# Kernel optimization log

Measured on AMD Instinct MI355X. Metric: run time of the kernel, lower is better.

The kernel has to match this reference:

```python
import jax, jax.numpy as jnp
import numpy as np

N_GENE = 4762
N_CELL = 847


def _graph_conv(x_src, src, dst, n_src, n_dst, W, b):
    """DGL GraphConv with norm='both': D_src^{-1/2} A D_dst^{-1/2} X W + b."""
    ones_e = jnp.ones(src.shape, jnp.float32)
    deg_out = jax.ops.segment_sum(ones_e, src, num_segments=n_src)
    norm_src = jnp.clip(deg_out, 1.0, None) ** -0.5
    feat = x_src * norm_src[:, None]            # [n_src, d]
    msg = feat[src]                              # gather  [E, d]
    agg = jax.ops.segment_sum(msg, dst, num_segments=n_dst)  # scatter-add [n_dst, d]
    deg_in = jax.ops.segment_sum(ones_e, dst, num_segments=n_dst)
    norm_dst = jnp.clip(deg_in, 1.0, None) ** -0.5
    return (agg * norm_dst[:, None]) @ W + b


def setup_inputs() -> dict:
    key = jax.random.key(0)
    ks = jax.random.split(key, 12)
    E = 200000
    d = 256
    inp = {
        "gene_emb": jax.random.normal(ks[0], (N_GENE, d), jnp.float32),
        "cell_emb": jax.random.normal(ks[1], (N_CELL, d), jnp.float32),
        "W_g2c": jax.random.normal(ks[2], (d, d), jnp.float32) * (1.0 / np.sqrt(d)),
        "b_g2c": jnp.zeros((d,), jnp.float32),
        "W_c2g": jax.random.normal(ks[3], (d, d), jnp.float32) * (1.0 / np.sqrt(d)),
        "b_c2g": jnp.zeros((d,), jnp.float32),
        "Wp": jax.random.normal(ks[4], (2 * d, 1), jnp.float32) * (1.0 / np.sqrt(2 * d)),
        "bp": jnp.zeros((1,), jnp.float32),
        "g2c_src": jax.random.randint(ks[5], (E,), 0, N_GENE, jnp.int32),
        "g2c_dst": jax.random.randint(ks[6], (E,), 0, N_CELL, jnp.int32),
        "c2g_src": jax.random.randint(ks[7], (E,), 0, N_CELL, jnp.int32),
        "c2g_dst": jax.random.randint(ks[8], (E,), 0, N_GENE, jnp.int32),
        "dec_src": jax.random.randint(ks[9], (E,), 0, N_GENE, jnp.int32),
        "dec_dst": jax.random.randint(ks[10], (E,), 0, N_CELL, jnp.int32),
    }
    return inp


def reference(gene_emb, cell_emb, W_g2c, b_g2c, W_c2g, b_c2g, Wp, bp,
              g2c_src, g2c_dst, c2g_src, c2g_dst, dec_src, dec_dst):
    # HeteroGraphConv (aggregate='sum'): each dst type receives from one relation here.
    h_cell = _graph_conv(gene_emb, g2c_src, g2c_dst, N_GENE, N_CELL, W_g2c, b_g2c)
    h_gene = _graph_conv(cell_emb, c2g_src, c2g_dst, N_CELL, N_GENE, W_c2g, b_c2g)
    h_gene = jax.nn.relu(h_gene)
    h_cell = jax.nn.relu(h_cell)
    # HeteroMLPPredictor: concat(src_h, dst_h) @ Wp + bp on dec_graph edges.
    x = jnp.concatenate([h_gene[dec_src], h_cell[dec_dst]], axis=1)  # [E_dec, 512]
    score = x @ Wp + bp                                               # [E_dec, 1]
    return (score, h_gene, h_cell)
```

## Files before the change

kernel.cpp:

```cpp
#include <hip/hip_runtime.h>

#define N_GENE 4762
#define N_CELL 847
#define NEDGE  200000
#define D      256
#define NPART  64

typedef __attribute__((ext_vector_type(8))) short short8;
typedef __attribute__((ext_vector_type(8))) unsigned short ushort8v;
typedef __attribute__((ext_vector_type(4))) float f32x4;

#define S_G_OUT 0
#define S_C_IN  (S_G_OUT + N_GENE)
#define S_C_OUT (S_C_IN + N_CELL)
#define S_G_IN  (S_C_OUT + N_CELL)
#define NBINS   (S_G_IN + N_GENE)

#define ALIGN8(x) (((x) + 7) & ~7)

#define A_DEG      0
#define A_NRM      (A_DEG + NBINS)
#define A_OFFS_C   (A_NRM + NBINS)
#define A_OFFS_G   (A_OFFS_C + N_CELL + 1)
#define A_SORT_C   ALIGN8(A_OFFS_G + N_GENE + 1)
#define A_SORT_G   (A_SORT_C + 2 * NEDGE)
#define A_PART     (A_SORT_G + 2 * NEDGE)
#define A_SG       (A_PART + NPART * NBINS)
#define A_SC       (A_SG + N_GENE)
#define A_GENE_BF  ALIGN8(A_SC + N_CELL)
#define A_CELL_BF  ALIGN8(A_GENE_BF + N_GENE * D / 2)
#define A_WT1_BF   ALIGN8(A_CELL_BF + N_CELL * D / 2)
#define A_WT2_BF   ALIGN8(A_WT1_BF + D * D / 2)
#define A_AGGC_BF  ALIGN8(A_WT2_BF + D * D / 2)
#define A_AGGG_BF  ALIGN8(A_AGGC_BF + N_CELL * D / 2)

__device__ __forceinline__ unsigned short f2bf(float f) {
    unsigned u = __float_as_uint(f);
    u = (u + 0x7FFFu + ((u >> 16) & 1u)) >> 16;
    return (unsigned short)u;
}
__device__ __forceinline__ float bf2f(unsigned short b) {
    return __uint_as_float(((unsigned)b) << 16);
}

__global__ __launch_bounds__(1024) void k_pre(
        const int* __restrict__ g2c_src, const int* __restrict__ g2c_dst,
        const int* __restrict__ c2g_src, const int* __restrict__ c2g_dst,
        const float* __restrict__ gene_emb, const float* __restrict__ cell_emb,
        const float* __restrict__ W_g2c, const float* __restrict__ W_c2g,
        int* __restrict__ partial,
        unsigned short* __restrict__ gene_bf, unsigned short* __restrict__ cell_bf,
        unsigned short* __restrict__ wt1, unsigned short* __restrict__ wt2,
        float* __restrict__ sg, float* __restrict__ sc) {
    __shared__ int sh[N_GENE];
    int B = blockIdx.x, T = threadIdx.x;
    if (B < 4 * NPART) {
        int grp = B >> 6, blk = B & (NPART - 1);
        const int* idx;
        int segbase, segn;
        if      (grp == 0) { idx = g2c_src; segbase = S_G_OUT; segn = N_GENE; }
        else if (grp == 1) { idx = g2c_dst; segbase = S_C_IN;  segn = N_CELL; }
        else if (grp == 2) { idx = c2g_src; segbase = S_C_OUT; segn = N_CELL; }
        else               { idx = c2g_dst; segbase = S_G_IN;  segn = N_GENE; }
        for (int j = T; j < segn; j += 1024) sh[j] = 0;
        __syncthreads();
        const int chunk = (NEDGE + NPART - 1) / NPART;
        int e0 = blk * chunk, e1 = min(NEDGE, e0 + chunk);
        for (int e = e0 + T; e < e1; e += 1024) atomicAdd(&sh[idx[e]], 1);
        __syncthreads();
        int* pp = partial + blk * NBINS + segbase;
        for (int j = T; j < segn; j += 1024) pp[j] = sh[j];
    } else {
        const int NG = N_GENE * D, NC = N_CELL * D, NW = D * D;
        const int total = NG + NC + 2 * NW;
        for (int i = (B - 4 * NPART) * 1024 + T; i < total; i += 64 * 1024) {
            if (i < NG) {
                gene_bf[i] = f2bf(gene_emb[i]);
            } else if (i < NG + NC) {
                int j = i - NG;
                cell_bf[j] = f2bf(cell_emb[j]);
            } else if (i < NG + NC + NW) {
                int j = i - NG - NC;
                wt1[j] = f2bf(W_g2c[(j & 255) * D + (j >> 8)]);
            } else {
                int j = i - NG - NC - NW;
                wt2[j] = f2bf(W_c2g[(j & 255) * D + (j >> 8)]);
            }
        }
        for (int i = (B - 4 * NPART) * 1024 + T; i < N_GENE + N_CELL; i += 64 * 1024) {
            if (i < N_GENE) sg[i] = 0.f; else sc[i - N_GENE] = 0.f;
        }
    }
}

__global__ void k_reduce(int* __restrict__ partial, int* __restrict__ deg,
                         float* __restrict__ nrm) {
    int j = blockIdx.x * blockDim.x + threadIdx.x;
    if (j < NBINS) {
        int s = 0;
        #pragma unroll
        for (int b0 = 0; b0 < NPART; b0 += 32) {
            int t[32];
            #pragma unroll
            for (int u = 0; u < 32; u++) t[u] = partial[(b0 + u) * NBINS + j];
            #pragma unroll
            for (int u = 0; u < 32; u++) { partial[(b0 + u) * NBINS + j] = s; s += t[u]; }
        }
        deg[j] = s;
        nrm[j] = rsqrtf(fmaxf((float)s, 1.0f));
    }
}

__global__ __launch_bounds__(1024) void k_scatter(
        const int* __restrict__ g2c_src, const int* __restrict__ g2c_dst,
        const int* __restrict__ c2g_src, const int* __restrict__ c2g_dst,
        const int* __restrict__ deg, const int* __restrict__ partial,
        const float* __restrict__ nrm,
        int* __restrict__ offsC, int* __restrict__ offsG,
        int2* __restrict__ sortC, int2* __restrict__ sortG) {
    __shared__ int soffs[N_GENE + 1];
    __shared__ int scur[N_GENE];
    __shared__ int wsum[16];
    int T = threadIdx.x, blk = blockIdx.x, dir = blockIdx.y;
    const int* src  = dir ? c2g_src : g2c_src;
    const int* dst  = dir ? c2g_dst : g2c_dst;
    const int* dgs  = dir ? deg + S_G_IN : deg + S_C_IN;
    const float* nsv = dir ? nrm + S_C_OUT : nrm + S_G_OUT;
    int seg         = dir ? S_G_IN : S_C_IN;
    int nb          = dir ? N_GENE : N_CELL;
    int* goffs      = dir ? offsG : offsC;
    int2* sorted    = dir ? sortG : sortC;
    int per = (nb + 1023) >> 10;
    int i0 = T * per, i1 = min(nb, i0 + per);
    int loc[5];
    int s = 0;
    for (int i = i0; i < i1; i++) { loc[i - i0] = s; s += dgs[i]; }
    int lane = T & 63, w = T >> 6;
    int t = s;
    #pragma unroll
    for (int off = 1; off < 64; off <<= 1) {
        int u = __shfl_up(t, off);
        if (lane >= off) t += u;
    }
    if (lane == 63) wsum[w] = t;
    __syncthreads();
    if (w == 0 && lane < 16) {
        int x = wsum[lane];
        #pragma unroll
        for (int off = 1; off < 16; off <<= 1) {
            int u = __shfl_up(x, off);
            if (lane >= off) x += u;
        }
        wsum[lane] = x;
    }
    __syncthreads();
    int wbase = w ? wsum[w - 1] : 0;
    int excl = wbase + t - s;
    for (int i = i0; i < i1; i++) soffs[i] = excl + loc[i - i0];
    if (T == 1023) soffs[nb] = excl + s;
    __syncthreads();
    if (blk == 0)
        for (int j = T; j <= nb; j += 1024) goffs[j] = soffs[j];
    const int* basep = partial + blk * NBINS + seg;
    for (int j = T; j < nb; j += 1024) scur[j] = soffs[j] + basep[j];
    __syncthreads();
    const int chunk = (NEDGE + NPART - 1) / NPART;
    int e0 = blk * chunk, e1 = min(NEDGE, e0 + chunk);
    for (int e = e0 + T; e < e1; e += 1024) {
        int d = dst[e], sv = src[e];
        float nv = nsv[sv];
        int pos = atomicAdd(&scur[d], 1);
        sorted[pos] = make_int2(sv, __float_as_int(nv));
    }
}

__global__ __launch_bounds__(256) void k_agg(
        const unsigned short* __restrict__ gene_bf,
        const unsigned short* __restrict__ cell_bf,
        const int2* __restrict__ sortC, const int2* __restrict__ sortG,
        const int* __restrict__ offsC, const int* __restrict__ offsG,
        const float* __restrict__ nrm,
        unsigned short* __restrict__ aggC, unsigned short* __restrict__ aggG) {
    __shared__ int   sidx[4][64];
    __shared__ float snrm[4][64];
    __shared__ float pacc[4][256];
    int w = threadIdx.x >> 6, lane = threadIdx.x & 63;
    int half = lane >> 5, li = lane & 31;
    int B = blockIdx.x;
    bool isCell = B < N_CELL;

    int e0, e1;
    const unsigned short* emb;
    const int2* sorted;
    int node;
    if (isCell) {
        node = B;
        int f0 = offsC[node], f1 = offsC[node + 1];
        int ne = f1 - f0, nw = (ne + 3) >> 2;
        e0 = f0 + w * nw; e1 = min(f1, e0 + nw);
        emb = gene_bf; sorted = sortC;
    } else {
        node = (B - N_CELL) * 4 + w;
        if (node >= N_GENE) return;
        e0 = offsG[node]; e1 = offsG[node + 1];
        emb = cell_bf; sorted = sortG;
    }

    float acc[8];
    #pragma unroll
    for (int c = 0; c < 8; c++) acc[c] = 0.f;

    for (int base = e0; base < e1; base += 64) {
        int n = min(64, e1 - base);
        if (lane < n) {
            int2 pr = sorted[base + lane];
            sidx[w][lane] = pr.x;
            snrm[w][lane] = __int_as_float(pr.y);
        }
        int i = 0;
        for (; 2 * i + 16 <= n; i += 8) {
            ushort8v v[8];
            float nv[8];
            #pragma unroll
            for (int k = 0; k < 8; k++) {
                int jj = 2 * i + 2 * k + half;
                v[k] = *(const ushort8v*)&emb[sidx[w][jj] * D + li * 8];
                nv[k] = snrm[w][jj];
            }
            #pragma unroll
            for (int c = 0; c < 8; c++) {
                float s0 = 0.f;
                #pragma unroll
                for (int k = 0; k < 8; k++) s0 += bf2f(v[k][c]) * nv[k];
                acc[c] += s0;
            }
        }
        for (; 2 * i + 8 <= n; i += 4) {
            int j0 = 2 * i + half, j1 = 2 * i + 2 + half;
            int j2 = 2 * i + 4 + half, j3 = 2 * i + 6 + half;
            ushort8v v0 = *(const ushort8v*)&emb[sidx[w][j0] * D + li * 8];
            ushort8v v1 = *(const ushort8v*)&emb[sidx[w][j1] * D + li * 8];
            ushort8v v2 = *(const ushort8v*)&emb[sidx[w][j2] * D + li * 8];
            ushort8v v3 = *(const ushort8v*)&emb[sidx[w][j3] * D + li * 8];
            float n0 = snrm[w][j0], n1 = snrm[w][j1];
            float n2 = snrm[w][j2], n3 = snrm[w][j3];
            #pragma unroll
            for (int c = 0; c < 8; c++)
                acc[c] += bf2f(v0[c]) * n0 + bf2f(v1[c]) * n1 +
                          bf2f(v2[c]) * n2 + bf2f(v3[c]) * n3;
        }
        int npair = (n + 1) >> 1;
        for (; i < npair; i++) {
            int jj = 2 * i + half;
            bool ok = jj < n;
            int idx = ok ? sidx[w][jj] : sidx[w][0];
            float nv = ok ? snrm[w][jj] : 0.f;
            ushort8v v = *(const ushort8v*)&emb[idx * D + li * 8];
            #pragma unroll
            for (int c = 0; c < 8; c++) acc[c] += bf2f(v[c]) * nv;
        }
    }
    #pragma unroll
    for (int c = 0; c < 8; c++) acc[c] += __shfl_xor(acc[c], 32);

    if (isCell) {
        if (half == 0) {
            #pragma unroll
            for (int c = 0; c < 8; c++) pacc[w][li * 8 + c] = acc[c];
        }
        __syncthreads();
        int T = threadIdx.x;
        float s2 = pacc[0][T] + pacc[1][T] + pacc[2][T] + pacc[3][T];
        aggC[node * D + T] = f2bf(s2 * nrm[S_C_IN + node]);
    } else {
        if (half == 0) {
            float ndv = nrm[S_G_IN + node];
            ushort8v o;
            #pragma unroll
            for (int c = 0; c < 8; c++) o[c] = f2bf(acc[c] * ndv);
            *(ushort8v*)&aggG[node * D + li * 8] = o;
        }
    }
}

__global__ __launch_bounds__(256) void k_gemm2(
        const unsigned short* __restrict__ aggC, const unsigned short* __restrict__ aggG,
        const unsigned short* __restrict__ wt1, const unsigned short* __restrict__ wt2,
        const float* __restrict__ b_g2c, const float* __restrict__ b_c2g,
        const float* __restrict__ Wp,
        float* __restrict__ hC, float* __restrict__ hG,
        float* __restrict__ sg, float* __restrict__ sc) {
    const int CT = (N_CELL + 15) / 16;
    const int GT = (N_GENE + 15) / 16;
    int wid = blockIdx.x * 4 + (threadIdx.x >> 6);
    if (wid >= (CT + GT) * 4) return;
    int tid = wid >> 2, nq = wid & 3;
    int n0 = nq * 64;
    bool isCell = tid < CT;
    int tile = isCell ? tid : tid - CT;
    int m0 = tile * 16;
    int M = isCell ? N_CELL : N_GENE;
    const unsigned short* A  = isCell ? aggC : aggG;
    const unsigned short* Wt = isCell ? wt1 : wt2;
    const float* bias = isCell ? b_g2c : b_c2g;
    const float* wp   = isCell ? Wp + D : Wp;
    float* H  = isCell ? hC : hG;
    float* sv = isCell ? sc : sg;
    int lane = threadIdx.x & 63;
    int l15 = lane & 15, quad = lane >> 4;
    int arow = m0 + l15;
    if (arow >= M) arow = M - 1;
    f32x4 acc[4];
    #pragma unroll
    for (int t = 0; t < 4; t++) acc[t] = (f32x4){0.f, 0.f, 0.f, 0.f};
    #pragma unroll
    for (int k0 = 0; k0 < D; k0 += 32) {
        short8 a = *(const short8*)&A[arow * D + k0 + quad * 8];
        #pragma unroll
        for (int t = 0; t < 4; t++) {
            short8 b = *(const short8*)&Wt[(n0 + t * 16 + l15) * D + k0 + quad * 8];
            acc[t] = __builtin_amdgcn_mfma_f32_16x16x32_bf16(a, b, acc[t], 0, 0, 0);
        }
    }
    float dot[4] = {0.f, 0.f, 0.f, 0.f};
    #pragma unroll
    for (int t = 0; t < 4; t++) {
        int col = n0 + t * 16 + l15;
        float bv = bias[col], wv = wp[col];
        #pragma unroll
        for (int r = 0; r < 4; r++) {
            int row = m0 + quad * 4 + r;
            float h = fmaxf(acc[t][r] + bv, 0.f);
            if (row < M) H[row * D + col] = h;
            dot[r] += h * wv;
        }
    }
    #pragma unroll
    for (int off = 1; off < 16; off <<= 1) {
        #pragma unroll
        for (int r = 0; r < 4; r++) dot[r] += __shfl_xor(dot[r], off);
    }
    if (l15 == 0) {
        #pragma unroll
        for (int r = 0; r < 4; r++) {
            int row = m0 + quad * 4 + r;
            if (row < M) atomicAdd(&sv[row], dot[r]);
        }
    }
}

__global__ void k_score(const int* __restrict__ dsrc, const int* __restrict__ ddst,
                        const float* __restrict__ sg, const float* __restrict__ sc,
                        const float* __restrict__ bp, float* __restrict__ out) {
    int i = blockIdx.x * blockDim.x + threadIdx.x;
    if (i < NEDGE) out[i] = sg[dsrc[i]] + sc[ddst[i]] + bp[0];
}

extern "C" void kernel_launch(void* const* d_in, const int* in_sizes, int n_in,
                              void* d_out, int out_size, void* d_ws, size_t ws_size,
                              hipStream_t stream) {
    const float* gene_emb = (const float*)d_in[0];
    const float* cell_emb = (const float*)d_in[1];
    const float* W_g2c    = (const float*)d_in[2];
    const float* b_g2c    = (const float*)d_in[3];
    const float* W_c2g    = (const float*)d_in[4];
    const float* b_c2g    = (const float*)d_in[5];
    const float* Wp       = (const float*)d_in[6];
    const float* bp       = (const float*)d_in[7];
    const int* g2c_src = (const int*)d_in[8];
    const int* g2c_dst = (const int*)d_in[9];
    const int* c2g_src = (const int*)d_in[10];
    const int* c2g_dst = (const int*)d_in[11];
    const int* dec_src = (const int*)d_in[12];
    const int* dec_dst = (const int*)d_in[13];

    int*   wsi = (int*)d_ws;
    float* wsf = (float*)d_ws;
    unsigned short* gene_bf = (unsigned short*)(wsi + A_GENE_BF);
    unsigned short* cell_bf = (unsigned short*)(wsi + A_CELL_BF);
    unsigned short* wt1     = (unsigned short*)(wsi + A_WT1_BF);
    unsigned short* wt2     = (unsigned short*)(wsi + A_WT2_BF);
    unsigned short* aggC    = (unsigned short*)(wsi + A_AGGC_BF);
    unsigned short* aggG    = (unsigned short*)(wsi + A_AGGG_BF);
    int2* sortC = (int2*)(wsi + A_SORT_C);
    int2* sortG = (int2*)(wsi + A_SORT_G);

    float* out = (float*)d_out;
    float* out_score = out;
    float* out_hgene = out + NEDGE;
    float* out_hcell = out + NEDGE + N_GENE * D;

    k_pre<<<4 * NPART + 64, 1024, 0, stream>>>(g2c_src, g2c_dst, c2g_src, c2g_dst,
                                               gene_emb, cell_emb, W_g2c, W_c2g,
                                               wsi + A_PART, gene_bf, cell_bf, wt1, wt2,
                                               wsf + A_SG, wsf + A_SC);
    k_reduce<<<(NBINS + 255) / 256, 256, 0, stream>>>(wsi + A_PART, wsi + A_DEG,
                                                      wsf + A_NRM);
    {
        dim3 grid(NPART, 2);
        k_scatter<<<grid, 1024, 0, stream>>>(g2c_src, g2c_dst, c2g_src, c2g_dst,
                                             wsi + A_DEG, wsi + A_PART, wsf + A_NRM,
                                             wsi + A_OFFS_C, wsi + A_OFFS_G,
                                             sortC, sortG);
    }
    k_agg<<<N_CELL + (N_GENE + 3) / 4, 256, 0, stream>>>(
        gene_bf, cell_bf, sortC, sortG, wsi + A_OFFS_C, wsi + A_OFFS_G,
        wsf + A_NRM, aggC, aggG);
    {
        const int CT = (N_CELL + 15) / 16, GT = (N_GENE + 15) / 16;
        k_gemm2<<<CT + GT, 256, 0, stream>>>(aggC, aggG, wt1, wt2,
                                             b_g2c, b_c2g, Wp,
                                             out_hcell, out_hgene,
                                             wsf + A_SG, wsf + A_SC);
    }
    k_score<<<(NEDGE + 255) / 256, 256, 0, stream>>>(dec_src, dec_dst,
                                                     wsf + A_SG, wsf + A_SC, bp, out_score);
}
```

Before: 140.7 us.

## Map one wave per cell node in aggregation, deepen gather unroll, vectorize bf16 cast

```diff
diff --git a/kernel.cpp b/kernel.cpp
--- a/kernel.cpp
+++ b/kernel.cpp
@@ -72,22 +72,31 @@
         for (int j = T; j < segn; j += 1024) pp[j] = sh[j];
     } else {
         const int NG = N_GENE * D, NC = N_CELL * D, NW = D * D;
-        const int total = NG + NC + 2 * NW;
-        for (int i = (B - 4 * NPART) * 1024 + T; i < total; i += 64 * 1024) {
-            if (i < NG) {
-                gene_bf[i] = f2bf(gene_emb[i]);
-            } else if (i < NG + NC) {
-                int j = i - NG;
-                cell_bf[j] = f2bf(cell_emb[j]);
-            } else if (i < NG + NC + NW) {
-                int j = i - NG - NC;
-                wt1[j] = f2bf(W_g2c[(j & 255) * D + (j >> 8)]);
+        int base = (B - 4 * NPART) * 1024 + T;
+        const int CH = (NG + NC) / 8;
+        for (int c = base; c < CH; c += 64 * 1024) {
+            const float* sp;
+            unsigned short* dp;
+            if (c < NG / 8) { sp = gene_emb + c * 8; dp = gene_bf + c * 8; }
+            else { int j = (c - NG / 8) * 8; sp = cell_emb + j; dp = cell_bf + j; }
+            f32x4 x0 = *(const f32x4*)sp;
+            f32x4 x1 = *(const f32x4*)(sp + 4);
+            ushort8v o;
+            o[0] = f2bf(x0[0]); o[1] = f2bf(x0[1]);
+            o[2] = f2bf(x0[2]); o[3] = f2bf(x0[3]);
+            o[4] = f2bf(x1[0]); o[5] = f2bf(x1[1]);
+            o[6] = f2bf(x1[2]); o[7] = f2bf(x1[3]);
+            *(ushort8v*)dp = o;
+        }
+        for (int i = base; i < 2 * NW; i += 64 * 1024) {
+            if (i < NW) {
+                wt1[i] = f2bf(W_g2c[(i & 255) * D + (i >> 8)]);
             } else {
-                int j = i - NG - NC - NW;
+                int j = i - NW;
                 wt2[j] = f2bf(W_c2g[(j & 255) * D + (j >> 8)]);
             }
         }
-        for (int i = (B - 4 * NPART) * 1024 + T; i < N_GENE + N_CELL; i += 64 * 1024) {
+        for (int i = base; i < N_GENE + N_CELL; i += 64 * 1024) {
             if (i < N_GENE) sg[i] = 0.f; else sc[i - N_GENE] = 0.f;
         }
     }
@@ -183,27 +192,27 @@
         unsigned short* __restrict__ aggC, unsigned short* __restrict__ aggG) {
     __shared__ int   sidx[4][64];
     __shared__ float snrm[4][64];
-    __shared__ float pacc[4][256];
+    const int CB = (N_CELL + 3) / 4;
     int w = threadIdx.x >> 6, lane = threadIdx.x & 63;
     int half = lane >> 5, li = lane & 31;
     int B = blockIdx.x;
-    bool isCell = B < N_CELL;
-
-    int e0, e1;
+    bool isCell = B < CB;
+
+    int e0, e1, node;
     const unsigned short* emb;
     const int2* sorted;
-    int node;
+    unsigned short* outp;
+    int nseg;
     if (isCell) {
-        node = B;
-        int f0 = offsC[node], f1 = offsC[node + 1];
-        int ne = f1 - f0, nw = (ne + 3) >> 2;
-        e0 = f0 + w * nw; e1 = min(f1, e0 + nw);
-        emb = gene_bf; sorted = sortC;
+        node = B * 4 + w;
+        if (node >= N_CELL) return;
+        e0 = offsC[node]; e1 = offsC[node + 1];
+        emb = gene_bf; sorted = sortC; outp = aggC; nseg = S_C_IN;
     } else {
-        node = (B - N_CELL) * 4 + w;
+        node = (B - CB) * 4 + w;
         if (node >= N_GENE) return;
         e0 = offsG[node]; e1 = offsG[node + 1];
-        emb = cell_bf; sorted = sortG;
+        emb = cell_bf; sorted = sortG; outp = aggG; nseg = S_G_IN;
     }
 
     float acc[8];
@@ -218,12 +227,29 @@
             snrm[w][lane] = __int_as_float(pr.y);
         }
         int i = 0;
+        for (; 2 * i + 32 <= n; i += 16) {
+            ushort8v v[16];
+            float nv[16];
+            #pragma unroll
+            for (int k = 0; k < 16; k++) {
+                int jj = 2 * (i + k) + half;
+                v[k] = *(const ushort8v*)&emb[sidx[w][jj] * D + li * 8];
+                nv[k] = snrm[w][jj];
+            }
+            #pragma unroll
+            for (int c = 0; c < 8; c++) {
+                float s0 = 0.f;
+                #pragma unroll
+                for (int k = 0; k < 16; k++) s0 += bf2f(v[k][c]) * nv[k];
+                acc[c] += s0;
+            }
+        }
         for (; 2 * i + 16 <= n; i += 8) {
             ushort8v v[8];
             float nv[8];
             #pragma unroll
             for (int k = 0; k < 8; k++) {
-                int jj = 2 * i + 2 * k + half;
+                int jj = 2 * (i + k) + half;
                 v[k] = *(const ushort8v*)&emb[sidx[w][jj] * D + li * 8];
                 nv[k] = snrm[w][jj];
             }
@@ -263,23 +289,12 @@
     #pragma unroll
     for (int c = 0; c < 8; c++) acc[c] += __shfl_xor(acc[c], 32);
 
-    if (isCell) {
-        if (half == 0) {
-            #pragma unroll
-            for (int c = 0; c < 8; c++) pacc[w][li * 8 + c] = acc[c];
-        }
-        __syncthreads();
-        int T = threadIdx.x;
-        float s2 = pacc[0][T] + pacc[1][T] + pacc[2][T] + pacc[3][T];
-        aggC[node * D + T] = f2bf(s2 * nrm[S_C_IN + node]);
-    } else {
-        if (half == 0) {
-            float ndv = nrm[S_G_IN + node];
-            ushort8v o;
-            #pragma unroll
-            for (int c = 0; c < 8; c++) o[c] = f2bf(acc[c] * ndv);
-            *(ushort8v*)&aggG[node * D + li * 8] = o;
-        }
+    if (half == 0) {
+        float ndv = nrm[nseg + node];
+        ushort8v o;
+        #pragma unroll
+        for (int c = 0; c < 8; c++) o[c] = f2bf(acc[c] * ndv);
+        *(ushort8v*)&outp[node * D + li * 8] = o;
     }
 }
 
@@ -403,9 +418,12 @@
                                              wsi + A_OFFS_C, wsi + A_OFFS_G,
                                              sortC, sortG);
     }
-    k_agg<<<N_CELL + (N_GENE + 3) / 4, 256, 0, stream>>>(
-        gene_bf, cell_bf, sortC, sortG, wsi + A_OFFS_C, wsi + A_OFFS_G,
-        wsf + A_NRM, aggC, aggG);
+    {
+        const int CB = (N_CELL + 3) / 4, GB = (N_GENE + 3) / 4;
+        k_agg<<<CB + GB, 256, 0, stream>>>(
+            gene_bf, cell_bf, sortC, sortG, wsi + A_OFFS_C, wsi + A_OFFS_G,
+            wsf + A_NRM, aggC, aggG);
+    }
     {
         const int CT = (N_CELL + 15) / 16, GT = (N_GENE + 15) / 16;
         k_gemm2<<<CT + GT, 256, 0, stream>>>(aggC, aggG, wt1, wt2,
```

After: 141.4 us. Within noise of the previous version (+0.5%).

## Fuse degree reduction into scatter kernel and vectorize bf16 embedding conversion

Applied to the files above, without the earlier changes.

```diff
diff --git a/kernel.cpp b/kernel.cpp
--- a/kernel.cpp
+++ b/kernel.cpp
@@ -18,8 +18,7 @@
 
 #define ALIGN8(x) (((x) + 7) & ~7)
 
-#define A_DEG      0
-#define A_NRM      (A_DEG + NBINS)
+#define A_NRM      0
 #define A_OFFS_C   (A_NRM + NBINS)
 #define A_OFFS_G   (A_OFFS_C + N_CELL + 1)
 #define A_SORT_C   ALIGN8(A_OFFS_G + N_GENE + 1)
@@ -72,69 +71,85 @@
         for (int j = T; j < segn; j += 1024) pp[j] = sh[j];
     } else {
         const int NG = N_GENE * D, NC = N_CELL * D, NW = D * D;
-        const int total = NG + NC + 2 * NW;
-        for (int i = (B - 4 * NPART) * 1024 + T; i < total; i += 64 * 1024) {
-            if (i < NG) {
-                gene_bf[i] = f2bf(gene_emb[i]);
-            } else if (i < NG + NC) {
-                int j = i - NG;
-                cell_bf[j] = f2bf(cell_emb[j]);
-            } else if (i < NG + NC + NW) {
-                int j = i - NG - NC;
-                wt1[j] = f2bf(W_g2c[(j & 255) * D + (j >> 8)]);
+        int base = (B - 4 * NPART) * 1024 + T;
+        const int CH = (NG + NC) / 8;
+        for (int c = base; c < CH; c += 64 * 1024) {
+            const float* sp;
+            unsigned short* dp;
+            if (c < NG / 8) { sp = gene_emb + c * 8; dp = gene_bf + c * 8; }
+            else { int j = (c - NG / 8) * 8; sp = cell_emb + j; dp = cell_bf + j; }
+            f32x4 x0 = *(const f32x4*)sp;
+            f32x4 x1 = *(const f32x4*)(sp + 4);
+            ushort8v o;
+            o[0] = f2bf(x0[0]); o[1] = f2bf(x0[1]);
+            o[2] = f2bf(x0[2]); o[3] = f2bf(x0[3]);
+            o[4] = f2bf(x1[0]); o[5] = f2bf(x1[1]);
+            o[6] = f2bf(x1[2]); o[7] = f2bf(x1[3]);
+            *(ushort8v*)dp = o;
+        }
+        for (int i = base; i < 2 * NW; i += 64 * 1024) {
+            if (i < NW) {
+                wt1[i] = f2bf(W_g2c[(i & 255) * D + (i >> 8)]);
             } else {
-                int j = i - NG - NC - NW;
+                int j = i - NW;
                 wt2[j] = f2bf(W_c2g[(j & 255) * D + (j >> 8)]);
             }
         }
-        for (int i = (B - 4 * NPART) * 1024 + T; i < N_GENE + N_CELL; i += 64 * 1024) {
+        for (int i = base; i < N_GENE + N_CELL; i += 64 * 1024) {
             if (i < N_GENE) sg[i] = 0.f; else sc[i - N_GENE] = 0.f;
         }
-    }
-}
-
-__global__ void k_reduce(int* __restrict__ partial, int* __restrict__ deg,
-                         float* __restrict__ nrm) {
-    int j = blockIdx.x * blockDim.x + threadIdx.x;
-    if (j < NBINS) {
-        int s = 0;
-        #pragma unroll
-        for (int b0 = 0; b0 < NPART; b0 += 32) {
-            int t[32];
-            #pragma unroll
-            for (int u = 0; u < 32; u++) t[u] = partial[(b0 + u) * NBINS + j];
-            #pragma unroll
-            for (int u = 0; u < 32; u++) { partial[(b0 + u) * NBINS + j] = s; s += t[u]; }
-        }
-        deg[j] = s;
-        nrm[j] = rsqrtf(fmaxf((float)s, 1.0f));
     }
 }
 
 __global__ __launch_bounds__(1024) void k_scatter(
         const int* __restrict__ g2c_src, const int* __restrict__ g2c_dst,
         const int* __restrict__ c2g_src, const int* __restrict__ c2g_dst,
-        const int* __restrict__ deg, const int* __restrict__ partial,
-        const float* __restrict__ nrm,
+        const int* __restrict__ partial, float* __restrict__ nrm,
         int* __restrict__ offsC, int* __restrict__ offsG,
         int2* __restrict__ sortC, int2* __restrict__ sortG) {
-    __shared__ int soffs[N_GENE + 1];
-    __shared__ int scur[N_GENE];
-    __shared__ int wsum[16];
+    __shared__ int   segbuf[N_GENE + N_CELL];
+    __shared__ int   srank[N_GENE];
+    __shared__ int   soffs[N_GENE + 1];
+    __shared__ int   wsum[16];
     int T = threadIdx.x, blk = blockIdx.x, dir = blockIdx.y;
     const int* src  = dir ? c2g_src : g2c_src;
     const int* dst  = dir ? c2g_dst : g2c_dst;
-    const int* dgs  = dir ? deg + S_G_IN : deg + S_C_IN;
-    const float* nsv = dir ? nrm + S_C_OUT : nrm + S_G_OUT;
     int seg         = dir ? S_G_IN : S_C_IN;
+    int sseg        = dir ? S_C_OUT : S_G_OUT;
     int nb          = dir ? N_GENE : N_CELL;
+    int ns          = dir ? N_CELL : N_GENE;
     int* goffs      = dir ? offsG : offsC;
     int2* sorted    = dir ? sortG : sortC;
+    int* stot       = segbuf;
+    float* nsrcf    = (float*)(segbuf + nb);
+
+    for (int j = T; j < nb; j += 1024) {
+        const int* pp = partial + seg + j;
+        int tot = 0, rank = 0;
+        #pragma unroll 8
+        for (int b = 0; b < NPART; b++) {
+            int v = pp[b * NBINS];
+            tot += v;
+            if (b < blk) rank += v;
+        }
+        stot[j] = tot;
+        srank[j] = rank;
+        if (blk == 0) nrm[seg + j] = rsqrtf(fmaxf((float)tot, 1.0f));
+    }
+    for (int j = T; j < ns; j += 1024) {
+        const int* pp = partial + sseg + j;
+        int tot = 0;
+        #pragma unroll 8
+        for (int b = 0; b < NPART; b++) tot += pp[b * NBINS];
+        nsrcf[j] = rsqrtf(fmaxf((float)tot, 1.0f));
+    }
+    __syncthreads();
+
     int per = (nb + 1023) >> 10;
     int i0 = T * per, i1 = min(nb, i0 + per);
     int loc[5];
     int s = 0;
-    for (int i = i0; i < i1; i++) { loc[i - i0] = s; s += dgs[i]; }
+    for (int i = i0; i < i1; i++) { loc[i - i0] = s; s += stot[i]; }
     int lane = T & 63, w = T >> 6;
     int t = s;
     #pragma unroll
@@ -161,15 +176,15 @@
     __syncthreads();
     if (blk == 0)
         for (int j = T; j <= nb; j += 1024) goffs[j] = soffs[j];
-    const int* basep = partial + blk * NBINS + seg;
-    for (int j = T; j < nb; j += 1024) scur[j] = soffs[j] + basep[j];
+    for (int j = T; j < nb; j += 1024) srank[j] += soffs[j];
     __syncthreads();
+
     const int chunk = (NEDGE + NPART - 1) / NPART;
     int e0 = blk * chunk, e1 = min(NEDGE, e0 + chunk);
     for (int e = e0 + T; e < e1; e += 1024) {
         int d = dst[e], sv = src[e];
-        float nv = nsv[sv];
-        int pos = atomicAdd(&scur[d], 1);
+        float nv = nsrcf[sv];
+        int pos = atomicAdd(&srank[d], 1);
         sorted[pos] = make_int2(sv, __float_as_int(nv));
     }
 }
@@ -394,12 +409,10 @@
                                                gene_emb, cell_emb, W_g2c, W_c2g,
                                                wsi + A_PART, gene_bf, cell_bf, wt1, wt2,
                                                wsf + A_SG, wsf + A_SC);
-    k_reduce<<<(NBINS + 255) / 256, 256, 0, stream>>>(wsi + A_PART, wsi + A_DEG,
-                                                      wsf + A_NRM);
     {
         dim3 grid(NPART, 2);
         k_scatter<<<grid, 1024, 0, stream>>>(g2c_src, g2c_dst, c2g_src, c2g_dst,
-                                             wsi + A_DEG, wsi + A_PART, wsf + A_NRM,
+                                             wsi + A_PART, wsf + A_NRM,
                                              wsi + A_OFFS_C, wsi + A_OFFS_G,
                                              sortC, sortG);
     }
```

Result: slower. 148.9 us (+5.8%).
